# Kernel optimization log

Measured on AMD Instinct MI355X. Metric: run time of the kernel, lower is better.

## Reference

```python
import jax, jax.numpy as jnp
import numpy as np

D = 1024
H = 16

def setup_inputs() -> dict:
    key = jax.random.key(0)
    k1, k2, k3 = jax.random.split(key, 3)
    B, T = 4, 2048
    x = jax.random.normal(k1, (B, T, D), dtype=jnp.float32)
    # Linear weights stored as [in, out] so y = x @ W (equivalent to torch Linear with weight.T)
    W_attn = jax.random.normal(k2, (D, 3 * D), dtype=jnp.float32) * (1.0 / np.sqrt(D))
    W_proj = jax.random.normal(k3, (D, D), dtype=jnp.float32) * (1.0 / np.sqrt(D))
    return {"x": x, "W_attn": W_attn, "W_proj": W_proj}

def reference(x, W_attn, W_proj):
    B, T, _ = x.shape
    hd = D // H  # head dim
    qkv = x @ W_attn  # [B,T,3D]
    q, k, v = jnp.split(qkv, 3, axis=-1)
    # [B,T,D] -> [B,H,T,hd]
    q = q.reshape(B, T, H, hd).transpose(0, 2, 1, 3)
    k = k.reshape(B, T, H, hd).transpose(0, 2, 1, 3)
    v = v.reshape(B, T, H, hd).transpose(0, 2, 1, 3)
    scale = 1.0 / np.sqrt(hd).astype(np.float32)
    att = jnp.einsum('bhqd,bhkd->bhqk', q, k) * scale  # [B,H,T,T]
    causal = jnp.tril(jnp.ones((T, T), dtype=bool))
    att = jnp.where(causal[None, None], att, jnp.finfo(att.dtype).min)
    att = jax.nn.softmax(att, axis=-1)
    y = jnp.einsum('bhqk,bhkd->bhqd', att, v)  # [B,H,T,hd]
    y = y.transpose(0, 2, 1, 3).reshape(B, T, D)
    return y @ W_proj
```

## Files before the change

### kernel.cpp

```cpp
#include <hip/hip_runtime.h>


typedef __bf16 bf16;
typedef __attribute__((ext_vector_type(8))) __bf16 bf16x8;
typedef __attribute__((ext_vector_type(4))) __bf16 bf16x4;
typedef __attribute__((ext_vector_type(4))) float f4;

#define BK 32

__device__ __forceinline__ void stage16(const bf16* g, bf16* l) {
    __builtin_amdgcn_global_load_lds((const __attribute__((address_space(1))) void*)g,
                                     (__attribute__((address_space(3))) void*)l,
                                     16, 0, 0);
}

__global__ __launch_bounds__(256)
void cast_f32_bf16(const float* __restrict__ src, bf16* __restrict__ dst, int n4)
{
    int i = blockIdx.x * 256 + threadIdx.x;
    if (i < n4) {
        float4 v = ((const float4*)src)[i];
        bf16x4 o = { (bf16)v.x, (bf16)v.y, (bf16)v.z, (bf16)v.w };
        *(bf16x4*)&dst[i * 4] = o;
    }
}

__global__ __launch_bounds__(256)
void transpose_f32_bf16(const float* __restrict__ src, bf16* __restrict__ dst,
                        int R, int C)
{
    __shared__ bf16 tile[64][65];
    int c0 = blockIdx.x * 64, r0 = blockIdx.y * 64;
    int tid = threadIdx.x;
    for (int i = tid; i < 64 * 64; i += 256) {
        int r = i >> 6, c = i & 63;
        tile[r][c] = (bf16)src[(long)(r0 + r) * C + c0 + c];
    }
    __syncthreads();
    for (int i = tid; i < 64 * 64; i += 256) {
        int r = i >> 6, c = i & 63;
        dst[(long)(c0 + r) * R + r0 + c] = tile[c][r];
    }
}

template <typename OutT>
__global__ __launch_bounds__(256)
void gemm_bt(const bf16* __restrict__ A, const bf16* __restrict__ Bt,
             OutT* __restrict__ C, int M, int N, int K, int lda, int ldc)
{
    __shared__ bf16 As[128 * BK];
    __shared__ bf16 Bs[128 * BK];
    int tid = threadIdx.x;
    int lane = tid & 63;
    int wid = tid >> 6;
    int wy = wid >> 1, wx = wid & 1;
    int m0 = blockIdx.y * 128, n0 = blockIdx.x * 128;

    f4 acc[4][4];
    #pragma unroll
    for (int mi = 0; mi < 4; ++mi)
        #pragma unroll
        for (int ni = 0; ni < 4; ++ni)
            acc[mi][ni] = (f4){0.f, 0.f, 0.f, 0.f};

    int srow = lane >> 2;
    int scol = (lane & 3) * 8;
    for (int kt = 0; kt < K; kt += BK) {
        #pragma unroll
        for (int i = 0; i < 2; ++i) {
            int chunk = wid * 2 + i;
            int row = chunk * 16 + srow;
            stage16(A  + (long)(m0 + row) * lda + kt + scol, As + chunk * 512 + lane * 8);
            stage16(Bt + (long)(n0 + row) * K   + kt + scol, Bs + chunk * 512 + lane * 8);
        }
        __syncthreads();
        bf16x8 af[4], bfr[4];
        #pragma unroll
        for (int mi = 0; mi < 4; ++mi)
            af[mi] = *(const bf16x8*)&As[(wy * 64 + mi * 16 + (lane & 15)) * BK + (lane >> 4) * 8];
        #pragma unroll
        for (int ni = 0; ni < 4; ++ni)
            bfr[ni] = *(const bf16x8*)&Bs[(wx * 64 + ni * 16 + (lane & 15)) * BK + (lane >> 4) * 8];
        #pragma unroll
        for (int mi = 0; mi < 4; ++mi)
            #pragma unroll
            for (int ni = 0; ni < 4; ++ni)
                acc[mi][ni] = __builtin_amdgcn_mfma_f32_16x16x32_bf16(af[mi], bfr[ni], acc[mi][ni], 0, 0, 0);
        __syncthreads();
    }
    #pragma unroll
    for (int mi = 0; mi < 4; ++mi) {
        int rbase = m0 + wy * 64 + mi * 16 + (lane >> 4) * 4;
        #pragma unroll
        for (int ni = 0; ni < 4; ++ni) {
            int col = n0 + wx * 64 + ni * 16 + (lane & 15);
            #pragma unroll
            for (int r = 0; r < 4; ++r)
                C[(long)(rbase + r) * ldc + col] = (OutT)acc[mi][ni][r];
        }
    }
}

#define QS 72
#define C_SL 0.18033688011112042f

__device__ __forceinline__ int vsw(int d, int k) {
    return d * 64 + ((((k >> 3) ^ (d & 7) ^ ((d >> 3) & 7)) & 7) << 3) + (k & 7);
}

__global__ __launch_bounds__(256)
void attn_mfma(bf16* __restrict__ qkv)
{
    __shared__ bf16 Ks[64 * QS];
    __shared__ bf16 Vt[64 * 64];
    __shared__ bf16 Ps[4 * 32 * QS];
    const int T = 2048, D3 = 3072;
    int tid = threadIdx.x;
    int lane = tid & 63, wid = tid >> 6;
    int quad = lane >> 4, col = lane & 15;
    int bh = blockIdx.x & 63;
    int qt = 15 - (blockIdx.x >> 6);
    int b = bh >> 4, h = bh & 15;
    long base = (long)b * T * D3 + h * 64;
    int q0 = qt * 128;
    int nk = 2 * qt + 2;
    int srow = tid >> 2, dseg = (tid & 3) * 16;
    bf16* Pw = &Ps[wid * 32 * QS];

    bf16x8 aq[2][2];
    #pragma unroll
    for (int nt = 0; nt < 2; ++nt) {
        const bf16* g = &qkv[base + (long)(q0 + wid * 32 + nt * 16 + col) * D3 + quad * 8];
        aq[nt][0] = *(const bf16x8*)g;
        aq[nt][1] = *(const bf16x8*)(g + 32);
    }
    bf16 one1 = (bf16)1.0f;
    bf16x8 bones = {one1, one1, one1, one1, one1, one1, one1, one1};

    f4 of[2][4], lac[2];
    #pragma unroll
    for (int mg = 0; mg < 2; ++mg) {
        lac[mg] = (f4){0.f, 0.f, 0.f, 0.f};
        #pragma unroll
        for (int n = 0; n < 4; ++n) of[mg][n] = (f4){0.f, 0.f, 0.f, 0.f};
    }

    const bf16* g0 = &qkv[base + (long)srow * D3 + 1024 + dseg];
    bf16x8 kr0 = *(const bf16x8*)g0;
    bf16x8 kr1 = *(const bf16x8*)(g0 + 8);
    bf16x8 vr0 = *(const bf16x8*)(g0 + 1024);
    bf16x8 vr1 = *(const bf16x8*)(g0 + 1032);

    for (int kt = 0; kt < nk; ++kt) {
        __syncthreads();
        *(bf16x8*)&Ks[srow * QS + dseg]     = kr0;
        *(bf16x8*)&Ks[srow * QS + dseg + 8] = kr1;
        #pragma unroll
        for (int j = 0; j < 8; ++j) {
            Vt[vsw(dseg + j, srow)]     = vr0[j];
            Vt[vsw(dseg + 8 + j, srow)] = vr1[j];
        }
        if (kt + 1 < nk) {
            const bf16* gn = &qkv[base + (long)((kt + 1) * 64 + srow) * D3 + 1024 + dseg];
            kr0 = *(const bf16x8*)gn;
            kr1 = *(const bf16x8*)(gn + 8);
            vr0 = *(const bf16x8*)(gn + 1024);
            vr1 = *(const bf16x8*)(gn + 1032);
        }
        __syncthreads();
        bool diag = (kt >= nk - 2);
        int k0 = kt * 64;
        #pragma unroll
        for (int mt = 0; mt < 4; ++mt) {
            bf16x8 ak0 = *(const bf16x8*)&Ks[(mt * 16 + col) * QS + quad * 8];
            bf16x8 ak1 = *(const bf16x8*)&Ks[(mt * 16 + col) * QS + 32 + quad * 8];
            #pragma unroll
            for (int nt = 0; nt < 2; ++nt) {
                f4 z = (f4){0.f, 0.f, 0.f, 0.f};
                __builtin_amdgcn_s_setprio(1);
                z = __builtin_amdgcn_mfma_f32_16x16x32_bf16(ak0, aq[nt][0], z, 0, 0, 0);
                f4 st = __builtin_amdgcn_mfma_f32_16x16x32_bf16(ak1, aq[nt][1], z, 0, 0, 0);
                __builtin_amdgcn_s_setprio(0);
                bf16x4 pk;
                if (diag) {
                    int qg = q0 + wid * 32 + nt * 16 + col;
                    #pragma unroll
                    for (int r = 0; r < 4; ++r) {
                        float arg = fmaf(st[r], C_SL, -16.f);
                        if ((k0 + mt * 16 + quad * 4 + r) > qg) arg = -1e30f;
                        pk[r] = (bf16)exp2f(arg);
                    }
                } else {
                    #pragma unroll
                    for (int r = 0; r < 4; ++r)
                        pk[r] = (bf16)exp2f(fmaf(st[r], C_SL, -16.f));
                }
                *(bf16x4*)&Pw[(nt * 16 + col) * QS + mt * 16 + quad * 4] = pk;
            }
        }
        bf16x8 ap[2][2];
        #pragma unroll
        for (int mg = 0; mg < 2; ++mg) {
            ap[mg][0] = *(const bf16x8*)&Pw[(mg * 16 + col) * QS + quad * 8];
            ap[mg][1] = *(const bf16x8*)&Pw[(mg * 16 + col) * QS + 32 + quad * 8];
        }
        #pragma unroll
        for (int nd = 0; nd < 4; ++nd) {
            bf16x8 bv0 = *(const bf16x8*)&Vt[vsw(nd * 16 + col, quad * 8)];
            bf16x8 bv1 = *(const bf16x8*)&Vt[vsw(nd * 16 + col, 32 + quad * 8)];
            __builtin_amdgcn_s_setprio(1);
            of[0][nd] = __builtin_amdgcn_mfma_f32_16x16x32_bf16(ap[0][0], bv0, of[0][nd], 0, 0, 0);
            of[0][nd] = __builtin_amdgcn_mfma_f32_16x16x32_bf16(ap[0][1], bv1, of[0][nd], 0, 0, 0);
            of[1][nd] = __builtin_amdgcn_mfma_f32_16x16x32_bf16(ap[1][0], bv0, of[1][nd], 0, 0, 0);
            of[1][nd] = __builtin_amdgcn_mfma_f32_16x16x32_bf16(ap[1][1], bv1, of[1][nd], 0, 0, 0);
            __builtin_amdgcn_s_setprio(0);
        }
        __builtin_amdgcn_s_setprio(1);
        #pragma unroll
        for (int mg = 0; mg < 2; ++mg) {
            lac[mg] = __builtin_amdgcn_mfma_f32_16x16x32_bf16(ap[mg][0], bones, lac[mg], 0, 0, 0);
            lac[mg] = __builtin_amdgcn_mfma_f32_16x16x32_bf16(ap[mg][1], bones, lac[mg], 0, 0, 0);
        }
        __builtin_amdgcn_s_setprio(0);
    }
    #pragma unroll
    for (int mg = 0; mg < 2; ++mg)
        #pragma unroll
        for (int r = 0; r < 4; ++r) {
            float inv = 1.f / lac[mg][r];
            long yoff = base + (long)(q0 + wid * 32 + mg * 16 + quad * 4 + r) * D3;
            #pragma unroll
            for (int nd = 0; nd < 4; ++nd)
                qkv[yoff + nd * 16 + col] = (bf16)(of[mg][nd][r] * inv);
        }
}

extern "C" void kernel_launch(void* const* d_in, const int* in_sizes, int n_in,
                              void* d_out, int out_size, void* d_ws, size_t ws_size,
                              hipStream_t stream) {
    const float* x      = (const float*)d_in[0];
    const float* W_attn = (const float*)d_in[1];
    const float* W_proj = (const float*)d_in[2];
    float* out = (float*)d_out;

    bf16* qkv = (bf16*)d_ws;
    bf16* WtA = qkv + (size_t)8192 * 3072;
    bf16* WtP = WtA + (size_t)3072 * 1024;
    bf16* xb = (bf16*)d_out;

    cast_f32_bf16<<<8192, 256, 0, stream>>>(x, xb, 8192 * 1024 / 4);
    transpose_f32_bf16<<<dim3(48, 16), 256, 0, stream>>>(W_attn, WtA, 1024, 3072);
    transpose_f32_bf16<<<dim3(16, 16), 256, 0, stream>>>(W_proj, WtP, 1024, 1024);
    gemm_bt<bf16><<<dim3(24, 64), 256, 0, stream>>>(xb, WtA, qkv, 8192, 3072,
                                                    1024, 1024, 3072);
    attn_mfma<<<1024, 256, 0, stream>>>(qkv);
    gemm_bt<float><<<dim3(8, 64), 256, 0, stream>>>(qkv, WtP, out, 8192, 1024,
                                                    1024, 3072, 1024);
}
```

Baseline: 266.4 us.

## Pair causal query tiles per attention block and swizzle GEMM block order

The attention kernel now gives each workgroup two query tiles, a short one (p) and a long one (15-p). Every block therefore does the same causal work, and the K/V tiles loaded for the short tile also feed the long tile. The grid drops to 512 blocks. V staging into the transposed LDS tile now uses 4x4 register transposes with vector LDS stores, replacing scalar scatter. The GEMM kernel also remaps block indices with an interleaved swizzle to change the L2 access pattern. The costs are higher register pressure from two sets of Q fragments and accumulators, and fewer blocks in flight.

```diff
diff --git a/kernel.cpp b/kernel.cpp
--- a/kernel.cpp
+++ b/kernel.cpp
@@ -54,7 +54,12 @@
     int lane = tid & 63;
     int wid = tid >> 6;
     int wy = wid >> 1, wx = wid & 1;
-    int m0 = blockIdx.y * 128, n0 = blockIdx.x * 128;
+
+    int nwg = gridDim.x * gridDim.y;
+    int bid = blockIdx.y * gridDim.x + blockIdx.x;
+    int swz = (bid & 7) * (nwg >> 3) + (bid >> 3);
+    int bx = swz % gridDim.x, by = swz / gridDim.x;
+    int m0 = by * 128, n0 = bx * 128;
 
     f4 acc[4][4];
     #pragma unroll
@@ -106,6 +111,84 @@
 
 __device__ __forceinline__ int vsw(int d, int k) {
     return d * 64 + ((((k >> 3) ^ (d & 7) ^ ((d >> 3) & 7)) & 7) << 3) + (k & 7);
+}
+
+__device__ __forceinline__ void attn_half(
+    const bf16x8 (&aq)[2][2], f4 (&of)[2][4], f4 (&lac)[2],
+    bf16* Pw, const bf16* Ks, const bf16* Vt,
+    int quad, int col, int q0w, int k0, bool diag)
+{
+    #pragma unroll
+    for (int mt = 0; mt < 4; ++mt) {
+        bf16x8 ak0 = *(const bf16x8*)&Ks[(mt * 16 + col) * QS + quad * 8];
+        bf16x8 ak1 = *(const bf16x8*)&Ks[(mt * 16 + col) * QS + 32 + quad * 8];
+        #pragma unroll
+        for (int nt = 0; nt < 2; ++nt) {
+            f4 z = (f4){0.f, 0.f, 0.f, 0.f};
+            __builtin_amdgcn_s_setprio(1);
+            z = __builtin_amdgcn_mfma_f32_16x16x32_bf16(ak0, aq[nt][0], z, 0, 0, 0);
+            f4 st = __builtin_amdgcn_mfma_f32_16x16x32_bf16(ak1, aq[nt][1], z, 0, 0, 0);
+            __builtin_amdgcn_s_setprio(0);
+            bf16x4 pk;
+            if (diag) {
+                int qg = q0w + nt * 16 + col;
+                #pragma unroll
+                for (int r = 0; r < 4; ++r) {
+                    float arg = fmaf(st[r], C_SL, -16.f);
+                    if ((k0 + mt * 16 + quad * 4 + r) > qg) arg = -1e30f;
+                    pk[r] = (bf16)exp2f(arg);
+                }
+            } else {
+                #pragma unroll
+                for (int r = 0; r < 4; ++r)
+                    pk[r] = (bf16)exp2f(fmaf(st[r], C_SL, -16.f));
+            }
+            *(bf16x4*)&Pw[(nt * 16 + col) * QS + mt * 16 + quad * 4] = pk;
+        }
+    }
+    bf16x8 ap[2][2];
+    #pragma unroll
+    for (int mg = 0; mg < 2; ++mg) {
+        ap[mg][0] = *(const bf16x8*)&Pw[(mg * 16 + col) * QS + quad * 8];
+        ap[mg][1] = *(const bf16x8*)&Pw[(mg * 16 + col) * QS + 32 + quad * 8];
+    }
+    #pragma unroll
+    for (int nd = 0; nd < 4; ++nd) {
+        bf16x8 bv0 = *(const bf16x8*)&Vt[vsw(nd * 16 + col, quad * 8)];
+        bf16x8 bv1 = *(const bf16x8*)&Vt[vsw(nd * 16 + col, 32 + quad * 8)];
+        __builtin_amdgcn_s_setprio(1);
+        of[0][nd] = __builtin_amdgcn_mfma_f32_16x16x32_bf16(ap[0][0], bv0, of[0][nd], 0, 0, 0);
+        of[0][nd] = __builtin_amdgcn_mfma_f32_16x16x32_bf16(ap[0][1], bv1, of[0][nd], 0, 0, 0);
+        of[1][nd] = __builtin_amdgcn_mfma_f32_16x16x32_bf16(ap[1][0], bv0, of[1][nd], 0, 0, 0);
+        of[1][nd] = __builtin_amdgcn_mfma_f32_16x16x32_bf16(ap[1][1], bv1, of[1][nd], 0, 0, 0);
+        __builtin_amdgcn_s_setprio(0);
+    }
+    bf16 one1 = (bf16)1.0f;
+    bf16x8 bones = {one1, one1, one1, one1, one1, one1, one1, one1};
+    __builtin_amdgcn_s_setprio(1);
+    #pragma unroll
+    for (int mg = 0; mg < 2; ++mg) {
+        lac[mg] = __builtin_amdgcn_mfma_f32_16x16x32_bf16(ap[mg][0], bones, lac[mg], 0, 0, 0);
+        lac[mg] = __builtin_amdgcn_mfma_f32_16x16x32_bf16(ap[mg][1], bones, lac[mg], 0, 0, 0);
+    }
+    __builtin_amdgcn_s_setprio(0);
+}
+
+__device__ __forceinline__ void attn_epi(
+    const f4 (&of)[2][4], const f4 (&lac)[2],
+    bf16* qkv, long base, int q0w, int quad, int col)
+{
+    const int D3 = 3072;
+    #pragma unroll
+    for (int mg = 0; mg < 2; ++mg)
+        #pragma unroll
+        for (int r = 0; r < 4; ++r) {
+            float inv = 1.f / lac[mg][r];
+            long yoff = base + (long)(q0w + mg * 16 + quad * 4 + r) * D3;
+            #pragma unroll
+            for (int nd = 0; nd < 4; ++nd)
+                qkv[yoff + nd * 16 + col] = (bf16)(of[mg][nd][r] * inv);
+        }
 }
 
 __global__ __launch_bounds__(256)
@@ -119,120 +202,91 @@
     int lane = tid & 63, wid = tid >> 6;
     int quad = lane >> 4, col = lane & 15;
     int bh = blockIdx.x & 63;
-    int qt = 15 - (blockIdx.x >> 6);
+    int p  = blockIdx.x >> 6;
     int b = bh >> 4, h = bh & 15;
     long base = (long)b * T * D3 + h * 64;
-    int q0 = qt * 128;
-    int nk = 2 * qt + 2;
+    int q0A = p * 128,        nkA = 2 * p + 2;
+    int q0B = (15 - p) * 128, nkB = 2 * (15 - p) + 2;
     int srow = tid >> 2, dseg = (tid & 3) * 16;
+    int kg = tid >> 4,  dg = tid & 15;
     bf16* Pw = &Ps[wid * 32 * QS];
-
-    bf16x8 aq[2][2];
+    int q0wA = q0A + wid * 32, q0wB = q0B + wid * 32;
+
+    bf16x8 aqA[2][2], aqB[2][2];
     #pragma unroll
     for (int nt = 0; nt < 2; ++nt) {
-        const bf16* g = &qkv[base + (long)(q0 + wid * 32 + nt * 16 + col) * D3 + quad * 8];
-        aq[nt][0] = *(const bf16x8*)g;
-        aq[nt][1] = *(const bf16x8*)(g + 32);
-    }
-    bf16 one1 = (bf16)1.0f;
-    bf16x8 bones = {one1, one1, one1, one1, one1, one1, one1, one1};
-
-    f4 of[2][4], lac[2];
+        const bf16* gA = &qkv[base + (long)(q0wA + nt * 16 + col) * D3 + quad * 8];
+        aqA[nt][0] = *(const bf16x8*)gA;
+        aqA[nt][1] = *(const bf16x8*)(gA + 32);
+        const bf16* gB = &qkv[base + (long)(q0wB + nt * 16 + col) * D3 + quad * 8];
+        aqB[nt][0] = *(const bf16x8*)gB;
+        aqB[nt][1] = *(const bf16x8*)(gB + 32);
+    }
+
+    f4 ofA[2][4], lacA[2], ofB[2][4], lacB[2];
     #pragma unroll
     for (int mg = 0; mg < 2; ++mg) {
-        lac[mg] = (f4){0.f, 0.f, 0.f, 0.f};
-        #pragma unroll
-        for (int n = 0; n < 4; ++n) of[mg][n] = (f4){0.f, 0.f, 0.f, 0.f};
-    }
-
-    const bf16* g0 = &qkv[base + (long)srow * D3 + 1024 + dseg];
-    bf16x8 kr0 = *(const bf16x8*)g0;
-    bf16x8 kr1 = *(const bf16x8*)(g0 + 8);
-    bf16x8 vr0 = *(const bf16x8*)(g0 + 1024);
-    bf16x8 vr1 = *(const bf16x8*)(g0 + 1032);
-
-    for (int kt = 0; kt < nk; ++kt) {
+        lacA[mg] = (f4){0.f, 0.f, 0.f, 0.f};
+        lacB[mg] = (f4){0.f, 0.f, 0.f, 0.f};
+        #pragma unroll
+        for (int n = 0; n < 4; ++n) {
+            ofA[mg][n] = (f4){0.f, 0.f, 0.f, 0.f};
+            ofB[mg][n] = (f4){0.f, 0.f, 0.f, 0.f};
+        }
+    }
+
+    const bf16* gK = &qkv[base + (long)srow * D3 + 1024 + dseg];
+    bf16x8 kr0 = *(const bf16x8*)gK;
+    bf16x8 kr1 = *(const bf16x8*)(gK + 8);
+    const bf16* gV = &qkv[base + (long)(kg * 4) * D3 + 2048 + dg * 4];
+    bf16x4 vr[4];
+    #pragma unroll
+    for (int j = 0; j < 4; ++j) vr[j] = *(const bf16x4*)(gV + (long)j * D3);
+
+    for (int kt = 0; kt < nkA; ++kt) {
         __syncthreads();
         *(bf16x8*)&Ks[srow * QS + dseg]     = kr0;
         *(bf16x8*)&Ks[srow * QS + dseg + 8] = kr1;
         #pragma unroll
-        for (int j = 0; j < 8; ++j) {
-            Vt[vsw(dseg + j, srow)]     = vr0[j];
-            Vt[vsw(dseg + 8 + j, srow)] = vr1[j];
-        }
-        if (kt + 1 < nk) {
-            const bf16* gn = &qkv[base + (long)((kt + 1) * 64 + srow) * D3 + 1024 + dseg];
-            kr0 = *(const bf16x8*)gn;
-            kr1 = *(const bf16x8*)(gn + 8);
-            vr0 = *(const bf16x8*)(gn + 1024);
-            vr1 = *(const bf16x8*)(gn + 1032);
-        }
-        __syncthreads();
-        bool diag = (kt >= nk - 2);
-        int k0 = kt * 64;
-        #pragma unroll
-        for (int mt = 0; mt < 4; ++mt) {
-            bf16x8 ak0 = *(const bf16x8*)&Ks[(mt * 16 + col) * QS + quad * 8];
-            bf16x8 ak1 = *(const bf16x8*)&Ks[(mt * 16 + col) * QS + 32 + quad * 8];
-            #pragma unroll
-            for (int nt = 0; nt < 2; ++nt) {
-                f4 z = (f4){0.f, 0.f, 0.f, 0.f};
-                __builtin_amdgcn_s_setprio(1);
-                z = __builtin_amdgcn_mfma_f32_16x16x32_bf16(ak0, aq[nt][0], z, 0, 0, 0);
-                f4 st = __builtin_amdgcn_mfma_f32_16x16x32_bf16(ak1, aq[nt][1], z, 0, 0, 0);
-                __builtin_amdgcn_s_setprio(0);
-                bf16x4 pk;
-                if (diag) {
-                    int qg = q0 + wid * 32 + nt * 16 + col;
-                    #pragma unroll
-                    for (int r = 0; r < 4; ++r) {
-                        float arg = fmaf(st[r], C_SL, -16.f);
-                        if ((k0 + mt * 16 + quad * 4 + r) > qg) arg = -1e30f;
-                        pk[r] = (bf16)exp2f(arg);
-                    }
-                } else {
-                    #pragma unroll
-                    for (int r = 0; r < 4; ++r)
-                        pk[r] = (bf16)exp2f(fmaf(st[r], C_SL, -16.f));
-                }
-                *(bf16x4*)&Pw[(nt * 16 + col) * QS + mt * 16 + quad * 4] = pk;
-            }
-        }
-        bf16x8 ap[2][2];
-        #pragma unroll
-        for (int mg = 0; mg < 2; ++mg) {
-            ap[mg][0] = *(const bf16x8*)&Pw[(mg * 16 + col) * QS + quad * 8];
-            ap[mg][1] = *(const bf16x8*)&Pw[(mg * 16 + col) * QS + 32 + quad * 8];
-        }
-        #pragma unroll
-        for (int nd = 0; nd < 4; ++nd) {
-            bf16x8 bv0 = *(const bf16x8*)&Vt[vsw(nd * 16 + col, quad * 8)];
-            bf16x8 bv1 = *(const bf16x8*)&Vt[vsw(nd * 16 + col, 32 + quad * 8)];
-            __builtin_amdgcn_s_setprio(1);
-            of[0][nd] = __builtin_amdgcn_mfma_f32_16x16x32_bf16(ap[0][0], bv0, of[0][nd], 0, 0, 0);
-            of[0][nd] = __builtin_amdgcn_mfma_f32_16x16x32_bf16(ap[0][1], bv1, of[0][nd], 0, 0, 0);
-            of[1][nd] = __builtin_amdgcn_mfma_f32_16x16x32_bf16(ap[1][0], bv0, of[1][nd], 0, 0, 0);
-            of[1][nd] = __builtin_amdgcn_mfma_f32_16x16x32_bf16(ap[1][1], bv1, of[1][nd], 0, 0, 0);
-            __builtin_amdgcn_s_setprio(0);
-        }
-        __builtin_amdgcn_s_setprio(1);
-        #pragma unroll
-        for (int mg = 0; mg < 2; ++mg) {
-            lac[mg] = __builtin_amdgcn_mfma_f32_16x16x32_bf16(ap[mg][0], bones, lac[mg], 0, 0, 0);
-            lac[mg] = __builtin_amdgcn_mfma_f32_16x16x32_bf16(ap[mg][1], bones, lac[mg], 0, 0, 0);
-        }
-        __builtin_amdgcn_s_setprio(0);
-    }
-    #pragma unroll
-    for (int mg = 0; mg < 2; ++mg)
-        #pragma unroll
-        for (int r = 0; r < 4; ++r) {
-            float inv = 1.f / lac[mg][r];
-            long yoff = base + (long)(q0 + wid * 32 + mg * 16 + quad * 4 + r) * D3;
-            #pragma unroll
-            for (int nd = 0; nd < 4; ++nd)
-                qkv[yoff + nd * 16 + col] = (bf16)(of[mg][nd][r] * inv);
-        }
+        for (int i = 0; i < 4; ++i) {
+            bf16x4 c = { vr[0][i], vr[1][i], vr[2][i], vr[3][i] };
+            *(bf16x4*)&Vt[vsw(dg * 4 + i, kg * 4)] = c;
+        }
+        {
+            const bf16* gKn = &qkv[base + (long)((kt + 1) * 64 + srow) * D3 + 1024 + dseg];
+            kr0 = *(const bf16x8*)gKn;
+            kr1 = *(const bf16x8*)(gKn + 8);
+            const bf16* gVn = &qkv[base + (long)((kt + 1) * 64 + kg * 4) * D3 + 2048 + dg * 4];
+            #pragma unroll
+            for (int j = 0; j < 4; ++j) vr[j] = *(const bf16x4*)(gVn + (long)j * D3);
+        }
+        __syncthreads();
+        attn_half(aqA, ofA, lacA, Pw, Ks, Vt, quad, col, q0wA, kt * 64, kt >= nkA - 2);
+        attn_half(aqB, ofB, lacB, Pw, Ks, Vt, quad, col, q0wB, kt * 64, false);
+    }
+    attn_epi(ofA, lacA, qkv, base, q0wA, quad, col);
+
+    for (int kt = nkA; kt < nkB; ++kt) {
+        __syncthreads();
+        *(bf16x8*)&Ks[srow * QS + dseg]     = kr0;
+        *(bf16x8*)&Ks[srow * QS + dseg + 8] = kr1;
+        #pragma unroll
+        for (int i = 0; i < 4; ++i) {
+            bf16x4 c = { vr[0][i], vr[1][i], vr[2][i], vr[3][i] };
+            *(bf16x4*)&Vt[vsw(dg * 4 + i, kg * 4)] = c;
+        }
+        if (kt + 1 < nkB) {
+            const bf16* gKn = &qkv[base + (long)((kt + 1) * 64 + srow) * D3 + 1024 + dseg];
+            kr0 = *(const bf16x8*)gKn;
+            kr1 = *(const bf16x8*)(gKn + 8);
+            const bf16* gVn = &qkv[base + (long)((kt + 1) * 64 + kg * 4) * D3 + 2048 + dg * 4];
+            #pragma unroll
+            for (int j = 0; j < 4; ++j) vr[j] = *(const bf16x4*)(gVn + (long)j * D3);
+        }
+        __syncthreads();
+        attn_half(aqB, ofB, lacB, Pw, Ks, Vt, quad, col, q0wB, kt * 64, kt >= nkB - 2);
+    }
+    attn_epi(ofB, lacB, qkv, base, q0wB, quad, col);
 }
 
 extern "C" void kernel_launch(void* const* d_in, const int* in_sizes, int n_in,
@@ -253,7 +307,7 @@
     transpose_f32_bf16<<<dim3(16, 16), 256, 0, stream>>>(W_proj, WtP, 1024, 1024);
     gemm_bt<bf16><<<dim3(24, 64), 256, 0, stream>>>(xb, WtA, qkv, 8192, 3072,
                                                     1024, 1024, 3072);
-    attn_mfma<<<1024, 256, 0, stream>>>(qkv);
+    attn_mfma<<<512, 256, 0, stream>>>(qkv);
     gemm_bt<float><<<dim3(8, 64), 256, 0, stream>>>(qkv, WtP, out, 8192, 1024,
                                                     1024, 3072, 1024);
 }
```

Result: slower. 274.1 us (+2.9%).
